# Performance work log

Hardware: AMD Instinct MI355X
Metric: run time of the kernel (lower is better)

Reference implementation:

```python
import jax, jax.numpy as jnp
import numpy as np

B, C, N, K, COUT, W32 = 4, 64, 4096, 16, 64, 32
EPS = 1e-5  # BatchNorm eps


def conv1x1(x, w, b):
    # x: (B, Cin, K, N), w: (Cout, Cin), b: (Cout,)
    return jnp.einsum('oi,bikn->bokn', w, x) + b[None, :, None, None]


def batchnorm(x, gamma, beta):
    # training-mode BN over (B, K, N) per channel
    m = x.mean(axis=(0, 2, 3), keepdims=True)
    v = x.var(axis=(0, 2, 3), keepdims=True)
    return gamma[None, :, None, None] * (x - m) * jax.lax.rsqrt(v + EPS) + beta[None, :, None, None]


def setup_inputs() -> dict:
    key = jax.random.key(0)
    ks = jax.random.split(key, 14)
    s = 0.1
    return {
        'inputs': jax.random.normal(ks[0], (B, C, N), jnp.float32),
        'inputs_pos': jax.random.normal(ks[1], (B, 3, N), jnp.float32),
        'inverse_density': jax.random.uniform(ks[2], (B, 1, N), jnp.float32),
        # WeightNet: Conv2d(3, 32, 1) + BN(32)
        'wn_w': jax.random.normal(ks[3], (W32, 3), jnp.float32) * s,
        'wn_b': jnp.zeros((W32,), jnp.float32),
        'wn_g': jnp.ones((W32,), jnp.float32),
        'wn_be': jnp.zeros((W32,), jnp.float32),
        # DensityNet: Conv2d(1,16,1)+BN(16), Conv2d(16,1,1)
        'dn_w1': jax.random.normal(ks[4], (16, 1), jnp.float32) * s,
        'dn_b1': jnp.zeros((16,), jnp.float32),
        'dn_g1': jnp.ones((16,), jnp.float32),
        'dn_be1': jnp.zeros((16,), jnp.float32),
        'dn_w2': jax.random.normal(ks[5], (1, 16), jnp.float32) * s,
        'dn_b2': jnp.zeros((1,), jnp.float32),
        # Linear(C*32, COUT)
        'lin_w': jax.random.normal(ks[6], (COUT, C * W32), jnp.float32) * (1.0 / np.sqrt(C * W32)),
        'lin_b': jnp.zeros((COUT,), jnp.float32),
    }


def reference(inputs, inputs_pos, inverse_density,
              wn_w, wn_b, wn_g, wn_be,
              dn_w1, dn_b1, dn_g1, dn_be1, dn_w2, dn_b2,
              lin_w, lin_b):
    b, c, n = inputs.shape
    # pairwise squared distances (B, N, N); stride=1 so no FPS sampling
    sq = jnp.sum(inputs_pos ** 2, axis=1)  # (B, N)
    dist = sq[:, :, None] + sq[:, None, :] - 2.0 * jnp.einsum('bdi,bdj->bij', inputs_pos, inputs_pos)
    _, nn_idx = jax.lax.top_k(-dist, K)  # (B, N, K) nearest neighbors (incl. self)

    def gather(x, idx):  # x: (Cx, N), idx: (N, K) -> (Cx, K, N)
        return jnp.transpose(x[:, idx], (0, 2, 1))

    nn_pos = jax.vmap(gather)(inputs_pos, nn_idx)        # (B, 3, K, N)
    nn_inputs = jax.vmap(gather)(inputs, nn_idx)         # (B, C, K, N)
    lnn_pos = nn_pos - inputs_pos[:, :, None, :]         # translated neighbor positions
    nn_inv_d = jax.vmap(gather)(inverse_density, nn_idx)  # (B, 1, K, N)

    density_scale = nn_inv_d / nn_inv_d.max(axis=2, keepdims=True)
    h = jax.nn.relu(batchnorm(conv1x1(density_scale, dn_w1, dn_b1), dn_g1, dn_be1))
    density_scale = jax.nn.sigmoid(conv1x1(h, dn_w2, dn_b2))  # (B, 1, K, N)

    scaled = nn_inputs * density_scale                    # (B, C, K, N)
    weights = jax.nn.relu(batchnorm(conv1x1(lnn_pos, wn_w, wn_b), wn_g, wn_be))  # (B, 32, K, N)

    # per-point matmul: (B,N,C,K) @ (B,N,K,32) -> (B,N,C,32)
    feat = jnp.einsum('bckn,bwkn->bncw', scaled, weights).reshape(b, n, c * W32)
    out = feat @ lin_w.T + lin_b                          # (B, N, COUT)
    return jnp.transpose(out, (0, 2, 1))                  # (B, COUT, N)
```

## Files before the change

kernel.cpp:

```cpp
#include <hip/hip_runtime.h>
#include <math.h>

#define NB 4
#define NC 64
#define NPTS 4096
#define NROWS (NB*NPTS)

typedef __attribute__((ext_vector_type(4))) float f32x4;
typedef __bf16 bf16x8 __attribute__((ext_vector_type(8)));

__device__ __forceinline__ ushort f2bf(float f) {
  unsigned u = __float_as_uint(f);
  u = (u + 0x7FFFu + ((u >> 16) & 1u)) >> 16;
  return (ushort)u;
}
__device__ __forceinline__ unsigned pk2(float lo, float hi) {
  return (unsigned)f2bf(lo) | ((unsigned)f2bf(hi) << 16);
}

__device__ __forceinline__ void insert16(double dist, int j, double (&dd)[16], int (&ii)[16]) {
  double cd = dist; int ci = j;
#pragma unroll
  for (int s = 0; s < 16; ++s) {
    double od = dd[s]; int oi = ii[s];
    bool c = cd < od;
    dd[s] = c ? cd : od;
    ii[s] = c ? ci : oi;
    cd = c ? od : cd;
    ci = c ? oi : ci;
  }
}

__device__ __forceinline__ void bub16u(unsigned key, unsigned (&t)[16]) {
#pragma unroll
  for (int q2 = 0; q2 < 16; ++q2) {
    unsigned lo = min(key, t[q2]);
    key = max(key, t[q2]);
    t[q2] = lo;
  }
}

__device__ __forceinline__ double wave_reduce(double v) {
#pragma unroll
  for (int off = 32; off; off >>= 1) v += __shfl_down(v, off, 64);
  return v;
}

__global__ __launch_bounds__(256) void pack_pos4(const float* __restrict__ pos,
                                                 float4* __restrict__ pos4) {
  int g = blockIdx.x * 256 + threadIdx.x;
  int b = g >> 12, n = g & (NPTS - 1);
  const float* pb = pos + b * 3 * NPTS;
  pos4[g] = make_float4(pb[n], pb[NPTS + n], pb[2 * NPTS + n], 0.f);
}

__global__ __launch_bounds__(256) void knn_sub(const float4* __restrict__ pos4,
                                               uint4* __restrict__ partials) {
  __shared__ float4 cand[128];
  int t = threadIdx.x;
  int row0 = blockIdx.x * 256;
  int b = row0 >> 12;
  int y = blockIdx.y;
  int j0 = (y >> 1) * 1024 + (y & 1) * 128;
  const float4* pb = pos4 + b * NPTS;
  if (t < 128) cand[t] = pb[j0 + t];
  __syncthreads();
  float4 q = pb[(row0 + t) & (NPTS - 1)];
  unsigned dd[16];
#pragma unroll
  for (int s = 0; s < 16; ++s) dd[s] = 0xFFFFFFFFu;
#pragma unroll 4
  for (int jj = 0; jj < 128; ++jj) {
    float4 c = cand[jj];
    float dx = q.x - c.x, dy = q.y - c.y, dz = q.z - c.z;
    float d = fmaf(dx, dx, fmaf(dy, dy, dz * dz));
    unsigned key = (__float_as_uint(d) & 0xFFFFF000u) | (unsigned)(j0 + jj);
#pragma unroll
    for (int s = 0; s < 16; ++s) {
      unsigned lo = min(key, dd[s]);
      key = max(key, dd[s]);
      dd[s] = lo;
    }
  }
  uint4* po = partials + ((size_t)y * NROWS + row0 + t) * 4;
  po[0] = make_uint4(dd[0], dd[1], dd[2], dd[3]);
  po[1] = make_uint4(dd[4], dd[5], dd[6], dd[7]);
  po[2] = make_uint4(dd[8], dd[9], dd[10], dd[11]);
  po[3] = make_uint4(dd[12], dd[13], dd[14], dd[15]);
}

__global__ __launch_bounds__(64) void knn_thresh(const uint4* __restrict__ partials,
                                                 unsigned* __restrict__ T0g) {
  __shared__ unsigned sl[64 * 132];
  int tid = threadIdx.x;
  int row0 = blockIdx.x * 64;
  uint4* sl4 = (uint4*)sl;
  size_t base = (size_t)row0 * 4 + tid;
#define TW(IT, V) { int g2 = ((IT) & 3) * 64 + tid; \
                    sl4[(g2 >> 2) * 33 + ((IT) >> 2) * 4 + (g2 & 3)] = (V); }
#define TB(B) { int IT0 = (B) * 8; \
  uint4 w0 = partials[(size_t)((IT0+0)>>2)*(NROWS*4) + ((IT0+0)&3)*64 + base]; \
  uint4 w1 = partials[(size_t)((IT0+1)>>2)*(NROWS*4) + ((IT0+1)&3)*64 + base]; \
  uint4 w2 = partials[(size_t)((IT0+2)>>2)*(NROWS*4) + ((IT0+2)&3)*64 + base]; \
  uint4 w3 = partials[(size_t)((IT0+3)>>2)*(NROWS*4) + ((IT0+3)&3)*64 + base]; \
  uint4 w4 = partials[(size_t)((IT0+4)>>2)*(NROWS*4) + ((IT0+4)&3)*64 + base]; \
  uint4 w5 = partials[(size_t)((IT0+5)>>2)*(NROWS*4) + ((IT0+5)&3)*64 + base]; \
  uint4 w6 = partials[(size_t)((IT0+6)>>2)*(NROWS*4) + ((IT0+6)&3)*64 + base]; \
  uint4 w7 = partials[(size_t)((IT0+7)>>2)*(NROWS*4) + ((IT0+7)&3)*64 + base]; \
  TW(IT0+0,w0) TW(IT0+1,w1) TW(IT0+2,w2) TW(IT0+3,w3) \
  TW(IT0+4,w4) TW(IT0+5,w5) TW(IT0+6,w6) TW(IT0+7,w7) }
  TB(0) TB(1) TB(2) TB(3)
#undef TB
#undef TW
  __syncthreads();
  unsigned top[16];
#pragma unroll
  for (int s = 0; s < 16; ++s) top[s] = 0xFFFFFFFFu;
  const unsigned* my = sl + tid * 132;
  for (int y = 0; y < 8; ++y) {
#pragma unroll 4
    for (int s = 0; s < 16; ++s) {
      unsigned key = my[y * 16 + s];
      if (key >= top[15]) break;
#pragma unroll
      for (int q2 = 0; q2 < 16; ++q2) {
        unsigned lo = min(key, top[q2]);
        key = max(key, top[q2]);
        top[q2] = lo;
      }
    }
  }
  T0g[row0 + tid] = top[15] & 0xFFFFF000u;
}

__global__ __launch_bounds__(256) void knn_filter(const float4* __restrict__ pos4,
                                                  const unsigned* __restrict__ T0g,
                                                  uint4* __restrict__ surv) {
  __shared__ float4 cand[256];
  __shared__ unsigned lq[256 * 28];
  int t = threadIdx.x;
  int row0 = blockIdx.x * 256;
  int b = row0 >> 12;
  int y = blockIdx.y;
  int j0 = y * 256;
  const float4* pb = pos4 + b * NPTS;
  cand[t] = pb[j0 + t];
  __syncthreads();
  int r = row0 + t;
  float4 q = pb[r & (NPTS - 1)];
  unsigned T = T0g[r];
  unsigned cnt = 0;
  unsigned* myq = lq + t * 28;
#pragma unroll 4
  for (int jj = 0; jj < 256; ++jj) {
    float4 c = cand[jj];
    float dx = q.x - c.x, dy = q.y - c.y, dz = q.z - c.z;
    float d = fmaf(dx, dx, fmaf(dy, dy, dz * dz));
    unsigned m = __float_as_uint(d) & 0xFFFFF000u;
    if (m <= T) {
      if (cnt < 28u) myq[cnt] = m | (unsigned)(j0 + jj);
      ++cnt;
    }
  }
  cnt = cnt < 28u ? cnt : 28u;
  unsigned t16[16];
#pragma unroll
  for (int s = 0; s < 16; ++s) t16[s] = 0xFFFFFFFFu;
  const uint4* qsrc = (const uint4*)myq;
  uint4 q0 = qsrc[0], q1 = qsrc[1], q2 = qsrc[2], q3 = qsrc[3],
        q4 = qsrc[4], q5 = qsrc[5], q6 = qsrc[6];
#define SIN(K, I) { unsigned key = ((I) < cnt) ? (K) : 0xFFFFFFFFu; bub16u(key, t16); }
  SIN(q0.x,0u) SIN(q0.y,1u) SIN(q0.z,2u) SIN(q0.w,3u)
  SIN(q1.x,4u) SIN(q1.y,5u) SIN(q1.z,6u) SIN(q1.w,7u)
  SIN(q2.x,8u) SIN(q2.y,9u) SIN(q2.z,10u) SIN(q2.w,11u)
  SIN(q3.x,12u) SIN(q3.y,13u) SIN(q3.z,14u) SIN(q3.w,15u)
  SIN(q4.x,16u) SIN(q4.y,17u) SIN(q4.z,18u) SIN(q4.w,19u)
  SIN(q5.x,20u) SIN(q5.y,21u) SIN(q5.z,22u) SIN(q5.w,23u)
  SIN(q6.x,24u) SIN(q6.y,25u) SIN(q6.z,26u) SIN(q6.w,27u)
#undef SIN
  uint4* dst = surv + ((size_t)r * 16 + y) * 4;
  dst[0] = make_uint4(t16[0], t16[1], t16[2], t16[3]);
  dst[1] = make_uint4(t16[4], t16[5], t16[6], t16[7]);
  dst[2] = make_uint4(t16[8], t16[9], t16[10], t16[11]);
  dst[3] = make_uint4(t16[12], t16[13], t16[14], t16[15]);
}

__global__ __launch_bounds__(256) void knn_final(const float4* __restrict__ pos4,
                                                 const float* __restrict__ invd,
                                                 const uint4* __restrict__ surv,
                                                 int* __restrict__ nn_idx,
                                                 float* __restrict__ dsbuf,
                                                 double* __restrict__ stp) {
  int t = threadIdx.x;
  int ln = t & 15;
  int r = blockIdx.x * 16 + (t >> 4);
  int b = r >> 12, n = r & (NPTS - 1);

  const uint4* sp = surv + ((size_t)r * 16 + ln) * 4;
  uint4 u0 = sp[0], u1 = sp[1], u2 = sp[2], u3 = sp[3];
  unsigned h0=u0.x,h1=u0.y,h2=u0.z,h3=u0.w,h4=u1.x,h5=u1.y,h6=u1.z,h7=u1.w,
           h8=u2.x,h9=u2.y,h10=u2.z,h11=u2.w,h12=u3.x,h13=u3.y,h14=u3.z,h15=u3.w;
  unsigned t0,t1,t2,t3,t4,t5,t6,t7,t8,t9,t10,t11,t12,t13,t14,t15,t16;
#define RND(TT) { unsigned m = h0; \
  m = min(m, (unsigned)__shfl_xor((int)m, 1)); \
  m = min(m, (unsigned)__shfl_xor((int)m, 2)); \
  m = min(m, (unsigned)__shfl_xor((int)m, 4)); \
  m = min(m, (unsigned)__shfl_xor((int)m, 8)); \
  TT = m; bool pop = (h0 == m); \
  h0 = pop ? h1 : h0;  h1 = pop ? h2 : h1;  h2 = pop ? h3 : h2; \
  h3 = pop ? h4 : h3;  h4 = pop ? h5 : h4;  h5 = pop ? h6 : h5; \
  h6 = pop ? h7 : h6;  h7 = pop ? h8 : h7;  h8 = pop ? h9 : h8; \
  h9 = pop ? h10 : h9; h10 = pop ? h11 : h10; h11 = pop ? h12 : h11; \
  h12 = pop ? h13 : h12; h13 = pop ? h14 : h13; h14 = pop ? h15 : h14; \
  h15 = pop ? 0xFFFFFFFFu : h15; }
  RND(t0) RND(t1) RND(t2) RND(t3) RND(t4) RND(t5) RND(t6) RND(t7)
  RND(t8) RND(t9) RND(t10) RND(t11) RND(t12) RND(t13) RND(t14) RND(t15)
  RND(t16)

  const float4* pb = pos4 + b * NPTS;
  float4 qp = pb[n];
  double xi = qp.x, yi = qp.y, zi = qp.z;

  int jm;
  bool tie = ((t15 & 0xFFFFF000u) == (t16 & 0xFFFFF000u));
  if (!tie) {
    unsigned tm = t0;
    tm = (ln == 1) ? t1 : tm;   tm = (ln == 2) ? t2 : tm;
    tm = (ln == 3) ? t3 : tm;   tm = (ln == 4) ? t4 : tm;
    tm = (ln == 5) ? t5 : tm;   tm = (ln == 6) ? t6 : tm;
    tm = (ln == 7) ? t7 : tm;   tm = (ln == 8) ? t8 : tm;
    tm = (ln == 9) ? t9 : tm;   tm = (ln == 10) ? t10 : tm;
    tm = (ln == 11) ? t11 : tm; tm = (ln == 12) ? t12 : tm;
    tm = (ln == 13) ? t13 : tm; tm = (ln == 14) ? t14 : tm;
    tm = (ln == 15) ? t15 : tm;
    jm = (int)(tm & 0xFFFu);
  } else {
    unsigned t17, t18, t19, t20, t21, t22, t23;
    RND(t17) RND(t18) RND(t19) RND(t20) RND(t21) RND(t22) RND(t23)
    double dd[16]; int ii[16];
#pragma unroll
    for (int s = 0; s < 16; ++s) { dd[s] = 1e300; ii[s] = 0; }
#define RRK(TT) if (TT != 0xFFFFFFFFu) { int j = (int)(TT & 0xFFFu); \
  float4 cj = pb[j]; \
  double dx = xi - (double)cj.x, dy = yi - (double)cj.y, dz = zi - (double)cj.z; \
  double dist = dx * dx + dy * dy + dz * dz; \
  if (dist < dd[15]) insert16(dist, j, dd, ii); }
    RRK(t0) RRK(t1) RRK(t2) RRK(t3) RRK(t4) RRK(t5) RRK(t6) RRK(t7)
    RRK(t8) RRK(t9) RRK(t10) RRK(t11) RRK(t12) RRK(t13) RRK(t14) RRK(t15)
    RRK(t16) RRK(t17) RRK(t18) RRK(t19) RRK(t20) RRK(t21) RRK(t22) RRK(t23)
#undef RRK
    int jj2 = ii[0];
#pragma unroll
    for (int s = 1; s < 16; ++s) jj2 = (ln == s) ? ii[s] : jj2;
    jm = jj2;
  }
#undef RND

  nn_idx[(size_t)r * 16 + ln] = jm;
  const float* ivb = invd + b * NPTS;
  float v = ivb[jm];
  float vmax = v;
  vmax = fmaxf(vmax, __shfl_xor(vmax, 1));
  vmax = fmaxf(vmax, __shfl_xor(vmax, 2));
  vmax = fmaxf(vmax, __shfl_xor(vmax, 4));
  vmax = fmaxf(vmax, __shfl_xor(vmax, 8));
  float x = v / vmax;
  dsbuf[(size_t)r * 16 + ln] = x;

  double sx = x, sxx = (double)x * (double)x;
  float4 pj = pb[jm];
  double lx = (double)pj.x - xi, lyv = (double)pj.y - yi, lzv = (double)pj.z - zi;
  double l1x = lx, l1y = lyv, l1z = lzv;
  double lxx = lx * lx, lyy = lyv * lyv, lzz = lzv * lzv;
  double lxy = lx * lyv, lxz = lx * lzv, lyz = lyv * lzv;
  sx  = wave_reduce(sx);  sxx = wave_reduce(sxx);
  l1x = wave_reduce(l1x); l1y = wave_reduce(l1y); l1z = wave_reduce(l1z);
  lxx = wave_reduce(lxx); lyy = wave_reduce(lyy); lzz = wave_reduce(lzz);
  lxy = wave_reduce(lxy); lxz = wave_reduce(lxz); lyz = wave_reduce(lyz);
  if ((t & 63) == 0) {
    double* o = stp + ((size_t)blockIdx.x * 4 + (t >> 6)) * 16;
    o[0] = sx;  o[1] = sxx;
    o[2] = l1x; o[3] = l1y; o[4] = l1z;
    o[5] = lxx; o[6] = lyy; o[7] = lzz;
    o[8] = lxy; o[9] = lxz; o[10] = lyz;
  }
}

__global__ __launch_bounds__(256) void finalize_params(const double* __restrict__ stp,
                                const float* __restrict__ wn_w,
                                const float* __restrict__ wn_g,
                                const float* __restrict__ wn_be,
                                const float* __restrict__ dn_w1,
                                const float* __restrict__ dn_g1,
                                const float* __restrict__ dn_be1,
                                float* __restrict__ prm) {
  __shared__ double part[16][16];
  __shared__ double red[11];
  const double M = (double)NROWS * 16.0;
  int t = threadIdx.x;
  {
    int c = t & 15, ch = t >> 4;
    double s = 0.0;
#pragma unroll 8
    for (int w = 0; w < 256; ++w) s += stp[(size_t)(ch * 256 + w) * 16 + c];
    part[ch][c] = s;
  }
  __syncthreads();
  if (t < 11) {
    double s = 0.0;
#pragma unroll
    for (int ch = 0; ch < 16; ++ch) s += part[ch][t];
    red[t] = s;
  }
  __syncthreads();
  if (t < 32) {
    double m0 = red[2] / M, m1 = red[3] / M, m2 = red[4] / M;
    double cxx = red[5] / M - m0 * m0, cyy = red[6] / M - m1 * m1, czz = red[7] / M - m2 * m2;
    double cxy = red[8] / M - m0 * m1, cxz = red[9] / M - m0 * m2, cyz = red[10] / M - m1 * m2;
    double w0 = wn_w[t * 3], w1 = wn_w[t * 3 + 1], w2 = wn_w[t * 3 + 2];
    double var = w0 * w0 * cxx + w1 * w1 * cyy + w2 * w2 * czz
               + 2.0 * (w0 * w1 * cxy + w0 * w2 * cxz + w1 * w2 * cyz);
    double alpha = (double)wn_g[t] / sqrt(var + 1e-5);
    double a0 = alpha * w0, a1 = alpha * w1, a2 = alpha * w2;
    prm[t * 3] = (float)a0; prm[t * 3 + 1] = (float)a1; prm[t * 3 + 2] = (float)a2;
    prm[96 + t] = (float)((double)wn_be[t] - (a0 * m0 + a1 * m1 + a2 * m2));
  } else if (t < 48) {
    int ch = t - 32;
    double mx = red[0] / M;
    double vx = red[1] / M - mx * mx;
    double w = dn_w1[ch];
    double alpha = (double)dn_g1[ch] * w / sqrt(w * w * vx + 1e-5);
    prm[128 + ch] = (float)alpha;
    prm[144 + ch] = (float)((double)dn_be1[ch] - alpha * mx);
  }
}

__global__ __launch_bounds__(256) void ds_kernel(float* __restrict__ dsbuf,
                                                 const float* __restrict__ prm,
                                                 const float* __restrict__ dn_w2,
                                                 const float* __restrict__ dn_b2) {
  int r = blockIdx.x * 256 + threadIdx.x;
  float A[16], Bp[16], W2[16];
#pragma unroll
  for (int ch = 0; ch < 16; ++ch) {
    A[ch] = prm[128 + ch];
    Bp[ch] = prm[144 + ch];
    W2[ch] = dn_w2[ch];
  }
  float b2 = dn_b2[0];
#pragma unroll
  for (int k = 0; k < 16; ++k) {
    float x = dsbuf[(size_t)r * 16 + k];
    float s = b2;
#pragma unroll
    for (int ch = 0; ch < 16; ++ch) s = fmaf(W2[ch], fmaxf(fmaf(A[ch], x, Bp[ch]), 0.f), s);
    dsbuf[(size_t)r * 16 + k] = 1.f / (1.f + expf(-s));
  }
}

__global__ __launch_bounds__(256) void transpose_in(const float* __restrict__ in,
                                                    ushort* __restrict__ inT) {
  __shared__ float tile[64][68];
  int t = threadIdx.x;
  int b = blockIdx.x >> 6;
  int n0 = (blockIdx.x & 63) << 6;
  {
    int c = t >> 2, q = t & 3;
    const float* src = in + ((size_t)(b * 64 + c)) * NPTS + n0 + q * 16;
    float4 v0 = ((const float4*)src)[0];
    float4 v1 = ((const float4*)src)[1];
    float4 v2 = ((const float4*)src)[2];
    float4 v3 = ((const float4*)src)[3];
    *(float4*)&tile[c][q * 16 + 0] = v0;
    *(float4*)&tile[c][q * 16 + 4] = v1;
    *(float4*)&tile[c][q * 16 + 8] = v2;
    *(float4*)&tile[c][q * 16 + 12] = v3;
  }
  __syncthreads();
  {
    int nl = t >> 2, cq = t & 3;
    unsigned pk[8];
#pragma unroll
    for (int i = 0; i < 8; ++i) {
      float lo = tile[cq * 16 + 2 * i][nl];
      float hi = tile[cq * 16 + 2 * i + 1][nl];
      pk[i] = pk2(lo, hi);
    }
    uint4* dst = (uint4*)(inT + ((size_t)(b * NPTS + n0 + nl)) * 64 + cq * 16);
    dst[0] = make_uint4(pk[0], pk[1], pk[2], pk[3]);
    dst[1] = make_uint4(pk[4], pk[5], pk[6], pk[7]);
  }
}

__global__ __launch_bounds__(256) void prep_LTf(const float* __restrict__ lin_w,
                                                ushort* __restrict__ LTf) {
  int g = blockIdx.x * 256 + threadIdx.x;
  int l = g & 63, ot = (g >> 6) & 3, s = g >> 8;
  int o = ot * 16 + (l & 15);
  const float* src = lin_w + (size_t)o * 2048 + s * 32 + (l >> 4) * 8;
  float4 u0 = ((const float4*)src)[0];
  float4 u1 = ((const float4*)src)[1];
  ((uint4*)LTf)[g] = make_uint4(pk2(u0.x, u0.y), pk2(u0.z, u0.w),
                                pk2(u1.x, u1.y), pk2(u1.z, u1.w));
}

#define XSTR 2320
#define WSTR 524

#define FMA_ROW(c) \
  a##c##_0 += W0 * (f32x4)x##c; a##c##_1 += W1 * (f32x4)x##c; \
  a##c##_2 += W2 * (f32x4)x##c; a##c##_3 += W3 * (f32x4)x##c; \
  a##c##_4 += W4 * (f32x4)x##c; a##c##_5 += W5 * (f32x4)x##c; \
  a##c##_6 += W6 * (f32x4)x##c; a##c##_7 += W7 * (f32x4)x##c;

#define WRITE_C(ci, csval) \
  { size_t base = ((size_t)(csval)) * 64 + pl; \
    aq[base +  0] = make_uint4(pk2(a##ci##_0.x, a##ci##_0.y), pk2(a##ci##_0.z, a##ci##_0.w), \
                               pk2(a##ci##_1.x, a##ci##_1.y), pk2(a##ci##_1.z, a##ci##_1.w)); \
    aq[base + 16] = make_uint4(pk2(a##ci##_2.x, a##ci##_2.y), pk2(a##ci##_2.z, a##ci##_2.w), \
                               pk2(a##ci##_3.x, a##ci##_3.y), pk2(a##ci##_3.z, a##ci##_3.w)); \
    aq[base + 32] = make_uint4(pk2(a##ci##_4.x, a##ci##_4.y), pk2(a##ci##_4.z, a##ci##_4.w), \
                               pk2(a##ci##_5.x, a##ci##_5.y), pk2(a##ci##_5.z, a##ci##_5.w)); \
    aq[base + 48] = make_uint4(pk2(a##ci##_6.x, a##ci##_6.y), pk2(a##ci##_6.z, a##ci##_6.w), \
                               pk2(a##ci##_7.x, a##ci##_7.y), pk2(a##ci##_7.z, a##ci##_7.w)); }

__global__ __launch_bounds__(256, 2) void fused(const ushort* __restrict__ inT,
                                                const float4* __restrict__ pos4,
                                                const int* __restrict__ nn_idx,
                                                const float* __restrict__ dsbuf,
                                                const float* __restrict__ prm_g,
                                                const ushort* __restrict__ LTf,
                                                const float* __restrict__ lin_b,
                                                float* __restrict__ out) {
  __shared__ __align__(16) char smem[16 * XSTR + 16 * WSTR * 4];
  __shared__ float prms[128];
  char* xraw = smem;
  float* wlds = (float*)(smem + 16 * XSTR);
  int t = threadIdx.x;
  int blk = blockIdx.x;
  int b = blk >> 8;
  int n0 = (blk & 255) << 4;
  if (t < 128) prms[t] = prm_g[t];
  __syncthreads();
  {
    int k = t >> 4, p = t & 15;
    int r = blk * 16 + p;
    int n = n0 + p;
    int j = nn_idx[(size_t)r * 16 + k];
    float4 pj = pos4[b * NPTS + j];
    float4 pn = pos4[b * NPTS + n];
    float lx = pj.x - pn.x, ly = pj.y - pn.y, lz = pj.z - pn.z;
    float ds = dsbuf[(size_t)r * 16 + k];
    const uint4* srcx = (const uint4*)(inT + ((size_t)(b * NPTS + j)) * 64);
    uint4* dstx = (uint4*)(xraw + p * XSTR + k * 144);
#pragma unroll
    for (int i = 0; i < 8; ++i) dstx[i] = srcx[i];
    float* wr = wlds + p * WSTR + k * 32;
#pragma unroll
    for (int w = 0; w < 32; ++w) {
      float v = fmaf(prms[w * 3], lx,
                fmaf(prms[w * 3 + 1], ly,
                fmaf(prms[w * 3 + 2], lz, prms[96 + w])));
      wr[w] = fmaxf(v, 0.f) * ds;
    }
  }
  __syncthreads();
  int pl = t & 15, cl = t >> 4;
  f32x4 a0_0=(f32x4)0.f, a0_1=(f32x4)0.f, a0_2=(f32x4)0.f, a0_3=(f32x4)0.f,
        a0_4=(f32x4)0.f, a0_5=(f32x4)0.f, a0_6=(f32x4)0.f, a0_7=(f32x4)0.f;
  f32x4 a1_0=(f32x4)0.f, a1_1=(f32x4)0.f, a1_2=(f32x4)0.f, a1_3=(f32x4)0.f,
        a1_4=(f32x4)0.f, a1_5=(f32x4)0.f, a1_6=(f32x4)0.f, a1_7=(f32x4)0.f;
  f32x4 a2_0=(f32x4)0.f, a2_1=(f32x4)0.f, a2_2=(f32x4)0.f, a2_3=(f32x4)0.f,
        a2_4=(f32x4)0.f, a2_5=(f32x4)0.f, a2_6=(f32x4)0.f, a2_7=(f32x4)0.f;
  f32x4 a3_0=(f32x4)0.f, a3_1=(f32x4)0.f, a3_2=(f32x4)0.f, a3_3=(f32x4)0.f,
        a3_4=(f32x4)0.f, a3_5=(f32x4)0.f, a3_6=(f32x4)0.f, a3_7=(f32x4)0.f;
  {
    const char* xrow = xraw + pl * XSTR;
    const float* wp = wlds + pl * WSTR;
#pragma unroll 4
    for (int kk = 0; kk < 16; ++kk) {
      unsigned xa = *(const unsigned*)(xrow + kk * 144 + cl * 4);
      unsigned xb = *(const unsigned*)(xrow + kk * 144 + 64 + cl * 4);
      float x0 = __uint_as_float(xa << 16);
      float x1 = __uint_as_float(xa & 0xFFFF0000u);
      float x2 = __uint_as_float(xb << 16);
      float x3 = __uint_as_float(xb & 0xFFFF0000u);
      const f32x4* wk = (const f32x4*)(wp + kk * 32);
      f32x4 W0 = wk[0], W1 = wk[1], W2 = wk[2], W3 = wk[3];
      f32x4 W4 = wk[4], W5 = wk[5], W6 = wk[6], W7 = wk[7];
      FMA_ROW(0)
      FMA_ROW(1)
      FMA_ROW(2)
      FMA_ROW(3)
    }
  }
  __syncthreads();
  uint4* aq = (uint4*)smem;
  WRITE_C(0, 2 * cl)
  WRITE_C(1, 2 * cl + 1)
  WRITE_C(2, 32 + 2 * cl)
  WRITE_C(3, 33 + 2 * cl)
  __syncthreads();
  {
    int wv = t >> 6, l = t & 63;
    const uint4* Lq = (const uint4*)LTf;
    f32x4 cacc = (f32x4)0.f;
#pragma unroll 4
    for (int s = 0; s < 64; ++s) {
      uint4 ua = aq[s * 64 + l];
      uint4 ub = Lq[(s * 4 + wv) * 64 + l];
      bf16x8 A = *reinterpret_cast<bf16x8*>(&ua);
      bf16x8 B = *reinterpret_cast<bf16x8*>(&ub);
      cacc = __builtin_amdgcn_mfma_f32_16x16x32_bf16(A, B, cacc, 0, 0, 0);
    }
    int o = wv * 16 + (l & 15);
    float bias = lin_b[o];
    cacc.x += bias; cacc.y += bias; cacc.z += bias; cacc.w += bias;
    *(f32x4*)(out + ((size_t)(b * 64 + o)) * NPTS + n0 + (l >> 4) * 4) = cacc;
  }
}

extern "C" void kernel_launch(void* const* d_in, const int* in_sizes, int n_in,
                              void* d_out, int out_size, void* d_ws, size_t ws_size,
                              hipStream_t stream) {
  (void)in_sizes; (void)n_in; (void)out_size; (void)ws_size;
  const float* inputs = (const float*)d_in[0];
  const float* pos    = (const float*)d_in[1];
  const float* invd   = (const float*)d_in[2];
  const float* wn_w   = (const float*)d_in[3];
  const float* wn_g   = (const float*)d_in[5];
  const float* wn_be  = (const float*)d_in[6];
  const float* dn_w1  = (const float*)d_in[7];
  const float* dn_g1  = (const float*)d_in[9];
  const float* dn_be1 = (const float*)d_in[10];
  const float* dn_w2  = (const float*)d_in[11];
  const float* dn_b2  = (const float*)d_in[12];
  const float* lin_w  = (const float*)d_in[13];
  const float* lin_b  = (const float*)d_in[14];
  float* outp = (float*)d_out;

  char* ws = (char*)d_ws;
  float*    prm      = (float*)(ws + 1024);
  float4*   pos4     = (float4*)(ws + 4096);
  int*      nnidx    = (int*)(ws + (size_t)(1u << 19));
  float*    dsbuf    = (float*)(ws + (size_t)(3u << 19));
  ushort*   inT      = (ushort*)(ws + (size_t)(5u << 19));
  ushort*   LTf      = (ushort*)(ws + (size_t)(9u << 19));
  unsigned* T0g      = (unsigned*)(ws + (size_t)(19u << 18));
  double*   stp      = (double*)(ws + (size_t)(5u << 20));
  uint4*    partials = (uint4*)(ws + (size_t)(11u << 19));
  uint4*    surv     = (uint4*)(ws + (size_t)(11u << 19));

  pack_pos4<<<64, 256, 0, stream>>>(pos, pos4);
  transpose_in<<<256, 256, 0, stream>>>(inputs, inT);
  prep_LTf<<<64, 256, 0, stream>>>(lin_w, LTf);
  knn_sub<<<dim3(64, 8), 256, 0, stream>>>(pos4, partials);
  knn_thresh<<<256, 64, 0, stream>>>(partials, T0g);
  knn_filter<<<dim3(64, 16), 256, 0, stream>>>(pos4, T0g, surv);
  knn_final<<<1024, 256, 0, stream>>>(pos4, invd, surv, nnidx, dsbuf, stp);
  finalize_params<<<1, 256, 0, stream>>>(stp, wn_w, wn_g, wn_be, dn_w1, dn_g1, dn_be1, prm);
  ds_kernel<<<64, 256, 0, stream>>>(dsbuf, prm, dn_w2, dn_b2);
  fused<<<1024, 256, 0, stream>>>(inT, pos4, nnidx, dsbuf, prm, LTf, lin_b, outp);
}
```

Baseline: 158.8 us.

## Compute per-point neighbor contraction with bf16 MFMA instead of FP32 FMAs

```diff
diff --git a/kernel.cpp b/kernel.cpp
--- a/kernel.cpp
+++ b/kernel.cpp
@@ -405,24 +405,8 @@
 }
 
 #define XSTR 2320
-#define WSTR 524
-
-#define FMA_ROW(c) \
-  a##c##_0 += W0 * (f32x4)x##c; a##c##_1 += W1 * (f32x4)x##c; \
-  a##c##_2 += W2 * (f32x4)x##c; a##c##_3 += W3 * (f32x4)x##c; \
-  a##c##_4 += W4 * (f32x4)x##c; a##c##_5 += W5 * (f32x4)x##c; \
-  a##c##_6 += W6 * (f32x4)x##c; a##c##_7 += W7 * (f32x4)x##c;
-
-#define WRITE_C(ci, csval) \
-  { size_t base = ((size_t)(csval)) * 64 + pl; \
-    aq[base +  0] = make_uint4(pk2(a##ci##_0.x, a##ci##_0.y), pk2(a##ci##_0.z, a##ci##_0.w), \
-                               pk2(a##ci##_1.x, a##ci##_1.y), pk2(a##ci##_1.z, a##ci##_1.w)); \
-    aq[base + 16] = make_uint4(pk2(a##ci##_2.x, a##ci##_2.y), pk2(a##ci##_2.z, a##ci##_2.w), \
-                               pk2(a##ci##_3.x, a##ci##_3.y), pk2(a##ci##_3.z, a##ci##_3.w)); \
-    aq[base + 32] = make_uint4(pk2(a##ci##_4.x, a##ci##_4.y), pk2(a##ci##_4.z, a##ci##_4.w), \
-                               pk2(a##ci##_5.x, a##ci##_5.y), pk2(a##ci##_5.z, a##ci##_5.w)); \
-    aq[base + 48] = make_uint4(pk2(a##ci##_6.x, a##ci##_6.y), pk2(a##ci##_6.z, a##ci##_6.w), \
-                               pk2(a##ci##_7.x, a##ci##_7.y), pk2(a##ci##_7.z, a##ci##_7.w)); }
+#define WTOFF 37120
+#define WTSTR 1552
 
 __global__ __launch_bounds__(256, 2) void fused(const ushort* __restrict__ inT,
                                                 const float4* __restrict__ pos4,
@@ -432,10 +416,10 @@
                                                 const ushort* __restrict__ LTf,
                                                 const float* __restrict__ lin_b,
                                                 float* __restrict__ out) {
-  __shared__ __align__(16) char smem[16 * XSTR + 16 * WSTR * 4];
+  __shared__ __align__(16) char smem[65536];
   __shared__ float prms[128];
   char* xraw = smem;
-  float* wlds = (float*)(smem + 16 * XSTR);
+  char* wT = smem + WTOFF;
   int t = threadIdx.x;
   int blk = blockIdx.x;
   int b = blk >> 8;
@@ -455,68 +439,109 @@
     uint4* dstx = (uint4*)(xraw + p * XSTR + k * 144);
 #pragma unroll
     for (int i = 0; i < 8; ++i) dstx[i] = srcx[i];
-    float* wr = wlds + p * WSTR + k * 32;
+    char* wr = wT + p * WTSTR + k * 2;
 #pragma unroll
     for (int w = 0; w < 32; ++w) {
       float v = fmaf(prms[w * 3], lx,
                 fmaf(prms[w * 3 + 1], ly,
                 fmaf(prms[w * 3 + 2], lz, prms[96 + w])));
-      wr[w] = fmaxf(v, 0.f) * ds;
+      *(ushort*)(wr + w * 48) = f2bf(fmaxf(v, 0.f) * ds);
     }
   }
   __syncthreads();
-  int pl = t & 15, cl = t >> 4;
-  f32x4 a0_0=(f32x4)0.f, a0_1=(f32x4)0.f, a0_2=(f32x4)0.f, a0_3=(f32x4)0.f,
-        a0_4=(f32x4)0.f, a0_5=(f32x4)0.f, a0_6=(f32x4)0.f, a0_7=(f32x4)0.f;
-  f32x4 a1_0=(f32x4)0.f, a1_1=(f32x4)0.f, a1_2=(f32x4)0.f, a1_3=(f32x4)0.f,
-        a1_4=(f32x4)0.f, a1_5=(f32x4)0.f, a1_6=(f32x4)0.f, a1_7=(f32x4)0.f;
-  f32x4 a2_0=(f32x4)0.f, a2_1=(f32x4)0.f, a2_2=(f32x4)0.f, a2_3=(f32x4)0.f,
-        a2_4=(f32x4)0.f, a2_5=(f32x4)0.f, a2_6=(f32x4)0.f, a2_7=(f32x4)0.f;
-  f32x4 a3_0=(f32x4)0.f, a3_1=(f32x4)0.f, a3_2=(f32x4)0.f, a3_3=(f32x4)0.f,
-        a3_4=(f32x4)0.f, a3_5=(f32x4)0.f, a3_6=(f32x4)0.f, a3_7=(f32x4)0.f;
+  int wv = t >> 6;
+  int l = t & 63;
+  int lr = l & 15;
+  int q = l >> 4;
+  int kq8 = (q & 1) * 1152;
+  int swz = (lr & 7) << 4;
+  const f32x4 zf = (f32x4)0.f;
+  uint4 zu = make_uint4(0u, 0u, 0u, 0u);
+
+#define DECLD(IT) unsigned d##IT##_0,d##IT##_1,d##IT##_2,d##IT##_3,d##IT##_4, \
+  d##IT##_5,d##IT##_6,d##IT##_7,d##IT##_8,d##IT##_9,d##IT##_10,d##IT##_11, \
+  d##IT##_12,d##IT##_13,d##IT##_14,d##IT##_15;
+  DECLD(0) DECLD(1) DECLD(2) DECLD(3)
+#undef DECLD
+
+#define LOADB(BU, NI, XP) { \
+    const char* xb = (XP) + ((NI) * 16 + lr) * 2; \
+    unsigned e0 = *(const ushort*)(xb); \
+    unsigned e1 = *(const ushort*)(xb + 144); \
+    unsigned e2 = *(const ushort*)(xb + 288); \
+    unsigned e3 = *(const ushort*)(xb + 432); \
+    unsigned e4 = *(const ushort*)(xb + 576); \
+    unsigned e5 = *(const ushort*)(xb + 720); \
+    unsigned e6 = *(const ushort*)(xb + 864); \
+    unsigned e7 = *(const ushort*)(xb + 1008); \
+    BU = make_uint4(e0 | (e1 << 16), e2 | (e3 << 16), \
+                    e4 | (e5 << 16), e6 | (e7 << 16)); }
+
+#define MM(AF, BF, RA, RB) { \
+    f32x4 D = __builtin_amdgcn_mfma_f32_16x16x32_bf16(AF, BF, zf, 0, 0, 0); \
+    RA = pk2(D.x, D.y); RB = pk2(D.z, D.w); }
+
+#define DO_POINT(IT) { \
+    int p = wv * 4 + (IT); \
+    const char* wtp = wT + p * WTSTR; \
+    const char* xp = xraw + p * XSTR + kq8; \
+    uint4 a0u = zu, a1u = zu; \
+    if (q < 2) { \
+      a0u = *(const uint4*)(wtp + lr * 48 + q * 16); \
+      a1u = *(const uint4*)(wtp + (16 + lr) * 48 + q * 16); \
+    } \
+    bf16x8 A0 = *reinterpret_cast<bf16x8*>(&a0u); \
+    bf16x8 A1 = *reinterpret_cast<bf16x8*>(&a1u); \
+    uint4 b0u, b1u, b2u, b3u; \
+    LOADB(b0u, 0, xp) LOADB(b1u, 1, xp) LOADB(b2u, 2, xp) LOADB(b3u, 3, xp) \
+    bf16x8 B0 = *reinterpret_cast<bf16x8*>(&b0u); \
+    bf16x8 B1 = *reinterpret_cast<bf16x8*>(&b1u); \
+    bf16x8 B2 = *reinterpret_cast<bf16x8*>(&b2u); \
+    bf16x8 B3 = *reinterpret_cast<bf16x8*>(&b3u); \
+    MM(A0, B0, d##IT##_0, d##IT##_1)   MM(A0, B1, d##IT##_2, d##IT##_3) \
+    MM(A0, B2, d##IT##_4, d##IT##_5)   MM(A0, B3, d##IT##_6, d##IT##_7) \
+    MM(A1, B0, d##IT##_8, d##IT##_9)   MM(A1, B1, d##IT##_10, d##IT##_11) \
+    MM(A1, B2, d##IT##_12, d##IT##_13) MM(A1, B3, d##IT##_14, d##IT##_15) }
+
+  DO_POINT(0) DO_POINT(1) DO_POINT(2) DO_POINT(3)
+#undef DO_POINT
+#undef MM
+#undef LOADB
+  __syncthreads();
   {
-    const char* xrow = xraw + pl * XSTR;
-    const float* wp = wlds + pl * WSTR;
-#pragma unroll 4
-    for (int kk = 0; kk < 16; ++kk) {
-      unsigned xa = *(const unsigned*)(xrow + kk * 144 + cl * 4);
-      unsigned xb = *(const unsigned*)(xrow + kk * 144 + 64 + cl * 4);
-      float x0 = __uint_as_float(xa << 16);
-      float x1 = __uint_as_float(xa & 0xFFFF0000u);
-      float x2 = __uint_as_float(xb << 16);
-      float x3 = __uint_as_float(xb & 0xFFFF0000u);
-      const f32x4* wk = (const f32x4*)(wp + kk * 32);
-      f32x4 W0 = wk[0], W1 = wk[1], W2 = wk[2], W3 = wk[3];
-      f32x4 W4 = wk[4], W5 = wk[5], W6 = wk[6], W7 = wk[7];
-      FMA_ROW(0)
-      FMA_ROW(1)
-      FMA_ROW(2)
-      FMA_ROW(3)
-    }
-  }
-  __syncthreads();
-  uint4* aq = (uint4*)smem;
-  WRITE_C(0, 2 * cl)
-  WRITE_C(1, 2 * cl + 1)
-  WRITE_C(2, 32 + 2 * cl)
-  WRITE_C(3, 33 + 2 * cl)
+    int hq = q >> 1;
+    int m0 = (q & 1) * 2;
+#define STT(IT, MI, NI, RA, RB) { \
+      int p = wv * 4 + (IT); \
+      int h = (MI) * 2 + hq; \
+      int base = ((NI) * 16 + lr) * 1024 + (p + 16 * h) * 16 + m0 * 4; \
+      *(unsigned*)(smem + (base ^ swz)) = RA; \
+      *(unsigned*)(smem + ((base + 4) ^ swz)) = RB; }
+#define STP(IT) \
+    STT(IT,0,0,d##IT##_0,d##IT##_1)   STT(IT,0,1,d##IT##_2,d##IT##_3) \
+    STT(IT,0,2,d##IT##_4,d##IT##_5)   STT(IT,0,3,d##IT##_6,d##IT##_7) \
+    STT(IT,1,0,d##IT##_8,d##IT##_9)   STT(IT,1,1,d##IT##_10,d##IT##_11) \
+    STT(IT,1,2,d##IT##_12,d##IT##_13) STT(IT,1,3,d##IT##_14,d##IT##_15)
+    STP(0) STP(1) STP(2) STP(3)
+#undef STP
+#undef STT
+  }
   __syncthreads();
   {
-    int wv = t >> 6, l = t & 63;
     const uint4* Lq = (const uint4*)LTf;
     f32x4 cacc = (f32x4)0.f;
 #pragma unroll 4
     for (int s = 0; s < 64; ++s) {
-      uint4 ua = aq[s * 64 + l];
+      uint4 ua = *(const uint4*)(smem + (((s * 64 + l) * 16) ^ ((s & 7) << 4)));
       uint4 ub = Lq[(s * 4 + wv) * 64 + l];
       bf16x8 A = *reinterpret_cast<bf16x8*>(&ua);
       bf16x8 B = *reinterpret_cast<bf16x8*>(&ub);
       cacc = __builtin_amdgcn_mfma_f32_16x16x32_bf16(A, B, cacc, 0, 0, 0);
     }
-    int o = wv * 16 + (l & 15);
+    int o = wv * 16 + lr;
     float bias = lin_b[o];
     cacc.x += bias; cacc.y += bias; cacc.z += bias; cacc.w += bias;
-    *(f32x4*)(out + ((size_t)(b * 64 + o)) * NPTS + n0 + (l >> 4) * 4) = cacc;
+    *(f32x4*)(out + ((size_t)(b * 64 + o)) * NPTS + n0 + q * 4) = cacc;
   }
 }
 
```

New measurement: 154.3 us. 2.8% less time.
